# Optimization experiments

Measured on AMD Instinct MI355X. Metric: run time of the kernel, lower is better.

## Reference

```python
import jax, jax.numpy as jnp
import numpy as np

B, N, D, H, C = 16, 512, 256, 8, 16
DK = D // H  # per-head dim


def gelu(x):
    return jax.nn.gelu(x, approximate=False)  # torch F.gelu default (erf)


def mha(x, Wq, Wk, Wv, Wo):
    # x: [N, D] treated as a length-N token sequence; standard scaled-dot MHA
    n = x.shape[0]
    q = (x @ Wq).reshape(n, H, DK)
    k = (x @ Wk).reshape(n, H, DK)
    v = (x @ Wv).reshape(n, H, DK)
    scores = jnp.einsum('nhd,mhd->hnm', q, k) / jnp.sqrt(jnp.asarray(DK, x.dtype))
    attn = jax.nn.softmax(scores, axis=-1)
    out = jnp.einsum('hnm,mhd->nhd', attn, v).reshape(n, H * DK)
    return out @ Wo


def setup_inputs() -> dict:
    key = jax.random.key(0)
    ks = jax.random.split(key, 16)
    scale = 1.0 / np.sqrt(D)
    w = lambda i, shape: jax.random.normal(ks[i], shape, jnp.float32) * scale
    return {
        'embeddings': jax.random.normal(ks[0], (B, N, D), jnp.float32),
        'labels': jax.random.randint(ks[1], (B, N), 0, C),
        'Wq0': w(2, (D, D)), 'Wk0': w(3, (D, D)), 'Wv0': w(4, (D, D)), 'Wo0': w(5, (D, D)),
        'Wq1': w(6, (D, D)), 'Wk1': w(7, (D, D)), 'Wv1': w(8, (D, D)), 'Wo1': w(9, (D, D)),
        'res_W': w(10, (D, D)), 'res_b': jnp.zeros((D,), jnp.float32),
        'ff_W1': w(11, (2 * D, D)), 'ff_b1': jnp.zeros((D,), jnp.float32),
        'ff_W2': w(12, (D, D)), 'ff_b2': jnp.zeros((D,), jnp.float32),
    }


def reference(embeddings, labels, Wq0, Wk0, Wv0, Wo0, Wq1, Wk1, Wv1, Wo1,
              res_W, res_b, ff_W1, ff_b1, ff_W2, ff_b2):
    # one-hot class membership; torch.unique over randint labels == arange(C)
    onehot = (labels[..., None] == jnp.arange(C)).astype(jnp.float32)  # [B,N,C]

    def episode(e, m):
        # e: [N, D]  m: [N, C]
        x = mha(e, Wq0, Wk0, Wv0, Wo0)
        x = gelu(x)
        x = mha(x, Wq1, Wk1, Wv1, Wo1)
        aggr = gelu(jnp.mean(x, axis=0))          # [D]  set-level summary
        aggr = aggr @ res_W + res_b               # res_linear
        e2 = jnp.concatenate([jnp.broadcast_to(aggr, (N, D)), e], axis=1)  # [N,2D]
        e2 = gelu(e2)
        e2 = gelu(e2 @ ff_W1 + ff_b1) @ ff_W2 + ff_b2  # ff_linear -> [N,D]
        # pairwise sample similarities with self-exclusion
        S = e2 @ e2.T                              # [N,N]
        S = S * (1.0 - jnp.eye(N, dtype=S.dtype))
        counts = jnp.sum(m, axis=0)                # [C]
        norm = counts[None, :] - m                 # leave-one-out class size [N,C]
        return (S.T @ m) / norm                    # per-class masked mean -> [N,C]

    return jax.vmap(episode)(embeddings, onehot)
```

## Files before the change

### kernel.cpp

```cpp
#include <hip/hip_runtime.h>

#define BB 16
#define NN 512
#define DD 256
#define HH 8
#define CC 16

typedef unsigned short u16;
using short8 = __attribute__((ext_vector_type(8))) short;
using f32x4  = __attribute__((ext_vector_type(4))) float;

__device__ __forceinline__ float gelu_f(float x) {
    return 0.5f * x * (1.0f + erff(x * 0.70710678118654752f));
}
__device__ __forceinline__ u16 f2bf(float f) {
    unsigned int u = __float_as_uint(f);
    unsigned int r = u + 0x7FFFu + ((u >> 16) & 1u);
    return (u16)(r >> 16);
}
__device__ __forceinline__ void gld16(const u16* g, const u16* l) {
    __builtin_amdgcn_global_load_lds(
        (const __attribute__((address_space(1))) unsigned int*)g,
        (__attribute__((address_space(3))) unsigned int*)l, 16, 0, 0);
}

#define QSCALE 0.25505412f

template<int ACT, int HAS_B, int HAS_T, int OUT_F32>
__global__ __launch_bounds__(256) void gemm64(
    const u16* __restrict__ A, const u16* __restrict__ W,
    u16* __restrict__ O, float* __restrict__ OF,
    const float* __restrict__ bias, const float* __restrict__ tvec)
{
    __shared__ __align__(16) u16 As[64 * 32];
    __shared__ __align__(16) u16 Bs[64 * 32];
    const int tid = threadIdx.x, wave = tid >> 6, lane = tid & 63;
    const int col = lane & 15, quad = lane >> 4;
    const int mbase = blockIdx.x * 64;
    const int nbase = blockIdx.y * 64;
    const int srow = lane >> 2, skk = (lane & 3) * 8;
    const int mh = (wave & 1) * 32, nh = (wave >> 1) * 32;

    f32x4 acc[2][2];
#pragma unroll
    for (int i = 0; i < 2; ++i)
#pragma unroll
        for (int j = 0; j < 2; ++j) acc[i][j] = (f32x4){0.f, 0.f, 0.f, 0.f};

    for (int k0 = 0; k0 < DD; k0 += 32) {
        gld16(A + (size_t)(mbase + wave * 16 + srow) * DD + k0 + skk, &As[wave * 512]);
        gld16(W + (size_t)(nbase + wave * 16 + srow) * DD + k0 + skk, &Bs[wave * 512]);
        __syncthreads();
        short8 af[2], bfr[2];
#pragma unroll
        for (int i = 0; i < 2; ++i) af[i]  = *(const short8*)&As[(mh + i * 16 + col) * 32 + quad * 8];
#pragma unroll
        for (int j = 0; j < 2; ++j) bfr[j] = *(const short8*)&Bs[(nh + j * 16 + col) * 32 + quad * 8];
#pragma unroll
        for (int i = 0; i < 2; ++i)
#pragma unroll
            for (int j = 0; j < 2; ++j)
                acc[i][j] = __builtin_amdgcn_mfma_f32_16x16x32_bf16(af[i], bfr[j], acc[i][j], 0, 0, 0);
        __syncthreads();
    }

    const int b = mbase >> 9;
#pragma unroll
    for (int i = 0; i < 2; ++i) {
#pragma unroll
        for (int j = 0; j < 2; ++j) {
            const int ccol = nbase + nh + j * 16 + col;
#pragma unroll
            for (int r = 0; r < 4; ++r) {
                const int crow = mbase + mh + i * 16 + quad * 4 + r;
                float v = acc[i][j][r];
                if (HAS_B) v += bias[ccol];
                if (HAS_T) v += tvec[b * DD + ccol];
                if (ACT)   v = gelu_f(v);
                if (OUT_F32) OF[(size_t)crow * DD + ccol] = v;
                else         O[(size_t)crow * DD + ccol] = f2bf(v);
            }
        }
    }
}

__global__ __launch_bounds__(256) void gemm_qkv(
    const u16* __restrict__ A,
    const u16* __restrict__ W0, const u16* __restrict__ W1, const u16* __restrict__ W2,
    u16* __restrict__ O0, u16* __restrict__ O1, u16* __restrict__ O2)
{
    __shared__ __align__(16) u16 As[64 * 32];
    __shared__ __align__(16) u16 Bs[64 * 32];
    const int tid = threadIdx.x, wave = tid >> 6, lane = tid & 63;
    const int col = lane & 15, quad = lane >> 4;
    const int mbase = blockIdx.x * 64;
    const int sel = blockIdx.y >> 2;
    const int nbase = (blockIdx.y & 3) * 64;
    const u16* W = (sel == 0) ? W0 : ((sel == 1) ? W1 : W2);
    u16* O = (sel == 0) ? O0 : ((sel == 1) ? O1 : O2);
    const int srow = lane >> 2, skk = (lane & 3) * 8;
    const int mh = (wave & 1) * 32, nh = (wave >> 1) * 32;

    f32x4 acc[2][2];
#pragma unroll
    for (int i = 0; i < 2; ++i)
#pragma unroll
        for (int j = 0; j < 2; ++j) acc[i][j] = (f32x4){0.f, 0.f, 0.f, 0.f};

    for (int k0 = 0; k0 < DD; k0 += 32) {
        gld16(A + (size_t)(mbase + wave * 16 + srow) * DD + k0 + skk, &As[wave * 512]);
        gld16(W + (size_t)(nbase + wave * 16 + srow) * DD + k0 + skk, &Bs[wave * 512]);
        __syncthreads();
        short8 af[2], bfr[2];
#pragma unroll
        for (int i = 0; i < 2; ++i) af[i]  = *(const short8*)&As[(mh + i * 16 + col) * 32 + quad * 8];
#pragma unroll
        for (int j = 0; j < 2; ++j) bfr[j] = *(const short8*)&Bs[(nh + j * 16 + col) * 32 + quad * 8];
#pragma unroll
        for (int i = 0; i < 2; ++i)
#pragma unroll
            for (int j = 0; j < 2; ++j)
                acc[i][j] = __builtin_amdgcn_mfma_f32_16x16x32_bf16(af[i], bfr[j], acc[i][j], 0, 0, 0);
        __syncthreads();
    }

    const int b = mbase >> 9;
#pragma unroll
    for (int i = 0; i < 2; ++i) {
#pragma unroll
        for (int j = 0; j < 2; ++j) {
            const int ccol = nbase + nh + j * 16 + col;
            const int tok0 = (mbase & 511) + mh + i * 16 + quad * 4;
            const int head = ccol >> 5, dk = ccol & 31;
            if (sel == 2) {
                ushort4 pk;
                pk.x = f2bf(acc[i][j][0]); pk.y = f2bf(acc[i][j][1]);
                pk.z = f2bf(acc[i][j][2]); pk.w = f2bf(acc[i][j][3]);
                *(ushort4*)&O[(((size_t)b * HH + head) * 32 + dk) * NN + tok0] = pk;
            } else {
#pragma unroll
                for (int r = 0; r < 4; ++r) {
                    float v = acc[i][j][r];
                    if (sel == 0) v *= QSCALE;
                    O[(((size_t)b * HH + head) * NN + tok0 + r) * 32 + dk] = f2bf(v);
                }
            }
        }
    }
}

template<int COLSUM>
__global__ __launch_bounds__(256) void attn_mfma(
    const u16* __restrict__ Qh, const u16* __restrict__ Kh,
    const u16* __restrict__ VT, u16* __restrict__ O,
    float* __restrict__ partial)
{
    __shared__ __align__(16) u16 Vt[32 * 520];
    __shared__ __align__(16) u16 Pc[4][16 * 32];
    __shared__ float cs[4][32];
    const int tid = threadIdx.x, wave = tid >> 6, lane = tid & 63;
    const int col = lane & 15, quad = lane >> 4;
    const int gid = blockIdx.x;
    const int qb = gid >> 7, bh = gid & 127;
    const int q0 = qb * 64 + wave * 16;

    const u16* vsrc = VT + (size_t)bh * 32 * NN;
#pragma unroll
    for (int i = 0; i < 8; ++i) {
        const int row = wave + i * 4;
        gld16(vsrc + (size_t)row * NN + lane * 8, &Vt[row * 520]);
    }
    const short8 aq = *(const short8*)(Qh + ((size_t)bh * NN + q0 + col) * 32 + quad * 8);
    __syncthreads();

    const u16* ksrc = Kh + (size_t)bh * NN * 32;
    float l[4] = {0.f, 0.f, 0.f, 0.f};
    f32x4 oacc[2];
    oacc[0] = (f32x4){0.f, 0.f, 0.f, 0.f};
    oacc[1] = (f32x4){0.f, 0.f, 0.f, 0.f};

    for (int g = 0; g < 16; ++g) {
#pragma unroll
        for (int k2 = 0; k2 < 2; ++k2) {
            const int kt = g * 2 + k2;
            const short8 bk = *(const short8*)(ksrc + (size_t)(kt * 16 + col) * 32 + quad * 8);
            f32x4 z = {0.f, 0.f, 0.f, 0.f};
            const f32x4 s = __builtin_amdgcn_mfma_f32_16x16x32_bf16(aq, bk, z, 0, 0, 0);
#pragma unroll
            for (int r = 0; r < 4; ++r) {
                const float p = exp2f(s[r]);
                l[r] += p;
                Pc[wave][(quad * 4 + r) * 32 + k2 * 16 + col] = f2bf(p);
            }
        }
        const short8 ap = *(const short8*)&Pc[wave][col * 32 + quad * 8];
#pragma unroll
        for (int nt = 0; nt < 2; ++nt) {
            const short8 bv = *(const short8*)&Vt[(nt * 16 + col) * 520 + g * 32 + quad * 8];
            oacc[nt] = __builtin_amdgcn_mfma_f32_16x16x32_bf16(ap, bv, oacc[nt], 0, 0, 0);
        }
    }
#pragma unroll
    for (int r = 0; r < 4; ++r) {
        l[r] += __shfl_xor(l[r], 1, 64);
        l[r] += __shfl_xor(l[r], 2, 64);
        l[r] += __shfl_xor(l[r], 4, 64);
        l[r] += __shfl_xor(l[r], 8, 64);
    }
    if (COLSUM) {
        float sv[2] = {0.f, 0.f};
#pragma unroll
        for (int nt = 0; nt < 2; ++nt) {
#pragma unroll
            for (int r = 0; r < 4; ++r) sv[nt] += oacc[nt][r] / l[r];
            sv[nt] += __shfl_xor(sv[nt], 16, 64);
            sv[nt] += __shfl_xor(sv[nt], 32, 64);
        }
        if (lane < 16) { cs[wave][col] = sv[0]; cs[wave][16 + col] = sv[1]; }
        __syncthreads();
        if (tid < 32)
            partial[(size_t)(bh * 8 + qb) * 32 + tid] =
                cs[0][tid] + cs[1][tid] + cs[2][tid] + cs[3][tid];
    } else {
        const int b = bh >> 3, h = bh & 7;
        u16* obase = O + ((size_t)b * NN) * DD + h * 32;
#pragma unroll
        for (int nt = 0; nt < 2; ++nt)
#pragma unroll
            for (int r = 0; r < 4; ++r)
                obase[(size_t)(q0 + quad * 4 + r) * DD + nt * 16 + col] = f2bf(oacc[nt][r] / l[r]);
    }
}

__global__ __launch_bounds__(256) void convert_all(
    const float* __restrict__ e, u16* __restrict__ E, u16* __restrict__ G,
    const float* s0, const float* s1, const float* s2, const float* s3,
    const float* s4, const float* s5, const float* s6, const float* s7,
    const float* s8, u16* __restrict__ Wt)
{
    const int bx = blockIdx.x;
    if (bx < 2048) {
        const size_t i = ((size_t)bx * 256 + threadIdx.x) * 4;
        const float4 v = *(const float4*)(e + i);
        ushort4 ev, gv;
        ev.x = f2bf(v.x); ev.y = f2bf(v.y); ev.z = f2bf(v.z); ev.w = f2bf(v.w);
        gv.x = f2bf(gelu_f(v.x)); gv.y = f2bf(gelu_f(v.y));
        gv.z = f2bf(gelu_f(v.z)); gv.w = f2bf(gelu_f(v.w));
        *(ushort4*)(E + i) = ev;
        *(ushort4*)(G + i) = gv;
    } else {
        const int w = bx - 2048;
        const int my = w >> 4, kb = (w & 15) * 16;
        const int n = threadIdx.x;
        const float* S;
        switch (my) {
            case 0: S = s0; break; case 1: S = s1; break; case 2: S = s2; break;
            case 3: S = s3; break; case 4: S = s4; break; case 5: S = s5; break;
            case 6: S = s6; break; case 7: S = s7; break; default: S = s8; break;
        }
        u16* Dst = Wt + (size_t)my * 65536;
        for (int r = 0; r < 16; ++r) {
            const int k = kb + r;
            Dst[(size_t)n * 256 + k] = f2bf(S[(size_t)k * 256 + n]);
        }
    }
}

__device__ __forceinline__ float mv256(const float* __restrict__ a,
                                       const float* __restrict__ W, int d)
{
    float acc[8] = {0.f, 0.f, 0.f, 0.f, 0.f, 0.f, 0.f, 0.f};
    for (int k = 0; k < 256; k += 8) {
#pragma unroll
        for (int j = 0; j < 8; ++j)
            acc[j] += a[k + j] * W[(size_t)(k + j) * 256 + d];
    }
    return ((acc[0] + acc[1]) + (acc[2] + acc[3])) + ((acc[4] + acc[5]) + (acc[6] + acc[7]));
}

__global__ __launch_bounds__(256) void aggr_v2(
    const float* __restrict__ partial, const float* __restrict__ Wo1f,
    const float* __restrict__ resW, const float* __restrict__ resb,
    const float* __restrict__ W1, const int* __restrict__ labels,
    float* __restrict__ tvec, float* __restrict__ counts)
{
    const int b = blockIdx.x, d = threadIdx.x;
    __shared__ float a0[256], a1[256], a2[256];
    __shared__ int hist[CC];
    if (d < CC) hist[d] = 0;
    const int h = d >> 5, d32 = d & 31;
    float s = 0.f;
#pragma unroll
    for (int qb = 0; qb < 8; ++qb)
        s += partial[(size_t)(((b * 8 + h) * 8) + qb) * 32 + d32];
    a0[d] = s * (1.0f / NN);
    __syncthreads();
    atomicAdd(&hist[labels[b * NN + d]], 1);
    atomicAdd(&hist[labels[b * NN + 256 + d]], 1);
    a1[d] = gelu_f(mv256(a0, Wo1f, d));
    __syncthreads();
    a2[d] = gelu_f(mv256(a1, resW, d) + resb[d]);
    __syncthreads();
    tvec[b * 256 + d] = mv256(a2, W1, d);
    if (d < CC) counts[b * CC + d] = (float)hist[d];
}

__global__ __launch_bounds__(256) void classsum_v2(
    const float* __restrict__ F, const int* __restrict__ labels,
    float* __restrict__ g)
{
    const int b = blockIdx.x, dch = blockIdx.y;
    const int t = threadIdx.x, w = t >> 6, lane = t & 63;
    __shared__ int lab[NN];
    __shared__ float gs[4][CC][64];
    lab[t] = labels[b * NN + t];
    lab[t + 256] = labels[b * NN + t + 256];
    __syncthreads();
    float acc[CC];
#pragma unroll
    for (int c = 0; c < CC; ++c) acc[c] = 0.f;
    const float* Fb = F + (size_t)b * NN * DD + dch * 64 + lane;
#pragma unroll 4
    for (int n = w * 128; n < w * 128 + 128; ++n) {
        const float v = Fb[(size_t)n * DD];
        const int lb = lab[n];
#pragma unroll
        for (int c = 0; c < CC; ++c) acc[c] += (lb == c) ? v : 0.f;
    }
#pragma unroll
    for (int c = 0; c < CC; ++c) gs[w][c][lane] = acc[c];
    __syncthreads();
#pragma unroll
    for (int i = 0; i < 4; ++i) {
        const int c = w * 4 + i;
        g[((size_t)b * CC + c) * DD + dch * 64 + lane] =
            gs[0][c][lane] + gs[1][c][lane] + gs[2][c][lane] + gs[3][c][lane];
    }
}

__global__ __launch_bounds__(256) void out_kernel(
    const float* __restrict__ F, const int* __restrict__ labels,
    const float* __restrict__ g, const float* __restrict__ counts,
    float* __restrict__ out)
{
    const int b = blockIdx.y;
    const int wave = threadIdx.x >> 6, lane = threadIdx.x & 63;
    const int n = blockIdx.x * 4 + wave;
    const float* fn = F + ((size_t)b * NN + n) * DD;
    const float* gb = g + (size_t)b * CC * DD;
    float fv[4];
#pragma unroll
    for (int i = 0; i < 4; ++i) fv[i] = fn[lane * 4 + i];
    float selfdot = 0.f;
#pragma unroll
    for (int i = 0; i < 4; ++i) selfdot += fv[i] * fv[i];
    float accs[CC];
#pragma unroll
    for (int c = 0; c < CC; ++c) {
        float sacc = 0.f;
#pragma unroll
        for (int i = 0; i < 4; ++i) sacc += fv[i] * gb[c * DD + lane * 4 + i];
        accs[c] = sacc;
    }
    for (int off = 32; off; off >>= 1) {
        selfdot += __shfl_xor(selfdot, off, 64);
#pragma unroll
        for (int c = 0; c < CC; ++c) accs[c] += __shfl_xor(accs[c], off, 64);
    }
    if (lane < CC) {
        const int c = lane;
        const int same = (labels[b * NN + n] == c) ? 1 : 0;
        const float num = accs[c] - (same ? selfdot : 0.f);
        const float den = counts[b * CC + c] - (float)same;
        out[((size_t)b * NN + n) * CC + c] = num / den;
    }
}

extern "C" void kernel_launch(void* const* d_in, const int* in_sizes, int n_in,
                              void* d_out, int out_size, void* d_ws, size_t ws_size,
                              hipStream_t stream)
{
    const float* emb    = (const float*)d_in[0];
    const int*   labels = (const int*)  d_in[1];
    const float* Wo1f = (const float*)d_in[9];
    const float* resW = (const float*)d_in[10];
    const float* resb = (const float*)d_in[11];
    const float* ffW1 = (const float*)d_in[12];
    const float* ffb1 = (const float*)d_in[13];
    const float* ffb2 = (const float*)d_in[15];
    float* out = (float*)d_out;

    const size_t SBE = (size_t)BB * NN * DD;
    u16* BUF0 = (u16*)d_ws;
    u16* BUF1 = BUF0 + SBE;
    u16* BUF2 = BUF1 + SBE;
    u16* BUF3 = BUF2 + SBE;
    u16* BUF4 = BUF3 + SBE;
    u16* BUF5 = BUF4 + SBE;
    u16* Wt   = BUF5 + SBE;
    float* F      = (float*)(Wt + 9 * 65536);
    float* tvec   = F + SBE;
    float* partial= tvec + BB * 256;
    float* gsum   = partial + 128 * 8 * 32;
    float* counts = gsum + (size_t)BB * CC * DD;

    convert_all<<<2048 + 144, 256, 0, stream>>>(
        emb, BUF0, BUF1,
        (const float*)d_in[2], (const float*)d_in[3], (const float*)d_in[4],
        (const float*)d_in[5], (const float*)d_in[6], (const float*)d_in[7],
        (const float*)d_in[8], ffW1 + 256 * 256, (const float*)d_in[14], Wt);
    gemm_qkv<<<dim3(128, 12), 256, 0, stream>>>(
        BUF0, Wt, Wt + 65536, Wt + 2 * 65536, BUF2, BUF3, BUF4);
    attn_mfma<0><<<1024, 256, 0, stream>>>(BUF2, BUF3, BUF4, BUF5, nullptr);
    gemm64<1,0,0,0><<<dim3(128, 4), 256, 0, stream>>>(
        BUF5, Wt + 3 * 65536, BUF0, nullptr, nullptr, nullptr);
    gemm_qkv<<<dim3(128, 12), 256, 0, stream>>>(
        BUF0, Wt + 4 * 65536, Wt + 5 * 65536, Wt + 6 * 65536, BUF2, BUF3, BUF4);
    attn_mfma<1><<<1024, 256, 0, stream>>>(BUF2, BUF3, BUF4, nullptr, partial);
    aggr_v2<<<BB, 256, 0, stream>>>(partial, Wo1f, resW, resb, ffW1, labels, tvec, counts);
    gemm64<1,1,1,0><<<dim3(128, 4), 256, 0, stream>>>(
        BUF1, Wt + 7 * 65536, BUF3, nullptr, ffb1, tvec);
    gemm64<0,1,0,1><<<dim3(128, 4), 256, 0, stream>>>(
        BUF3, Wt + 8 * 65536, nullptr, F, ffb2, nullptr);
    classsum_v2<<<dim3(BB, 4), 256, 0, stream>>>(F, labels, gsum);
    out_kernel<<<dim3(128, BB), 256, 0, stream>>>(F, labels, gsum, counts, out);
}
```

Before: 211.2 us.

## Fuse embedding conversion into GEMM loaders, widen QKV tiles, drop V LDS staging

The standalone embedding fp32→bf16 and gelu conversion pass is removed. The first QKV GEMM now converts fp32 embeddings while loading them, and the FF1 GEMM applies gelu plus the bf16 conversion in its A-tile loader. The QKV GEMM tile grows to 128 rows to reuse each weight tile across more rows. Attention reads V straight from global memory instead of staging it in LDS, pads the P buffer and adds an occupancy bound, which trades LDS use for more global/L2 traffic.

```diff
diff --git a/kernel.cpp b/kernel.cpp
--- a/kernel.cpp
+++ b/kernel.cpp
@@ -26,98 +26,66 @@
 
 #define QSCALE 0.25505412f
 
-template<int ACT, int HAS_B, int HAS_T, int OUT_F32>
-__global__ __launch_bounds__(256) void gemm64(
-    const u16* __restrict__ A, const u16* __restrict__ W,
-    u16* __restrict__ O, float* __restrict__ OF,
-    const float* __restrict__ bias, const float* __restrict__ tvec)
-{
-    __shared__ __align__(16) u16 As[64 * 32];
+template<int AFP32>
+__global__ __launch_bounds__(256) void gemm_qkv128(
+    const void* __restrict__ Av,
+    const u16* __restrict__ W0, const u16* __restrict__ W1, const u16* __restrict__ W2,
+    u16* __restrict__ O0, u16* __restrict__ O1, u16* __restrict__ O2)
+{
+    __shared__ __align__(16) u16 As[128 * 32];
     __shared__ __align__(16) u16 Bs[64 * 32];
     const int tid = threadIdx.x, wave = tid >> 6, lane = tid & 63;
     const int col = lane & 15, quad = lane >> 4;
-    const int mbase = blockIdx.x * 64;
-    const int nbase = blockIdx.y * 64;
-    const int srow = lane >> 2, skk = (lane & 3) * 8;
-    const int mh = (wave & 1) * 32, nh = (wave >> 1) * 32;
-
-    f32x4 acc[2][2];
-#pragma unroll
-    for (int i = 0; i < 2; ++i)
-#pragma unroll
-        for (int j = 0; j < 2; ++j) acc[i][j] = (f32x4){0.f, 0.f, 0.f, 0.f};
-
-    for (int k0 = 0; k0 < DD; k0 += 32) {
-        gld16(A + (size_t)(mbase + wave * 16 + srow) * DD + k0 + skk, &As[wave * 512]);
-        gld16(W + (size_t)(nbase + wave * 16 + srow) * DD + k0 + skk, &Bs[wave * 512]);
-        __syncthreads();
-        short8 af[2], bfr[2];
-#pragma unroll
-        for (int i = 0; i < 2; ++i) af[i]  = *(const short8*)&As[(mh + i * 16 + col) * 32 + quad * 8];
-#pragma unroll
-        for (int j = 0; j < 2; ++j) bfr[j] = *(const short8*)&Bs[(nh + j * 16 + col) * 32 + quad * 8];
-#pragma unroll
-        for (int i = 0; i < 2; ++i)
-#pragma unroll
-            for (int j = 0; j < 2; ++j)
-                acc[i][j] = __builtin_amdgcn_mfma_f32_16x16x32_bf16(af[i], bfr[j], acc[i][j], 0, 0, 0);
-        __syncthreads();
-    }
-
-    const int b = mbase >> 9;
-#pragma unroll
-    for (int i = 0; i < 2; ++i) {
-#pragma unroll
-        for (int j = 0; j < 2; ++j) {
-            const int ccol = nbase + nh + j * 16 + col;
-#pragma unroll
-            for (int r = 0; r < 4; ++r) {
-                const int crow = mbase + mh + i * 16 + quad * 4 + r;
-                float v = acc[i][j][r];
-                if (HAS_B) v += bias[ccol];
-                if (HAS_T) v += tvec[b * DD + ccol];
-                if (ACT)   v = gelu_f(v);
-                if (OUT_F32) OF[(size_t)crow * DD + ccol] = v;
-                else         O[(size_t)crow * DD + ccol] = f2bf(v);
-            }
-        }
-    }
-}
-
-__global__ __launch_bounds__(256) void gemm_qkv(
-    const u16* __restrict__ A,
-    const u16* __restrict__ W0, const u16* __restrict__ W1, const u16* __restrict__ W2,
-    u16* __restrict__ O0, u16* __restrict__ O1, u16* __restrict__ O2)
-{
-    __shared__ __align__(16) u16 As[64 * 32];
-    __shared__ __align__(16) u16 Bs[64 * 32];
-    const int tid = threadIdx.x, wave = tid >> 6, lane = tid & 63;
-    const int col = lane & 15, quad = lane >> 4;
-    const int mbase = blockIdx.x * 64;
+    const int mbase = blockIdx.x * 128;
     const int sel = blockIdx.y >> 2;
     const int nbase = (blockIdx.y & 3) * 64;
     const u16* W = (sel == 0) ? W0 : ((sel == 1) ? W1 : W2);
     u16* O = (sel == 0) ? O0 : ((sel == 1) ? O1 : O2);
     const int srow = lane >> 2, skk = (lane & 3) * 8;
-    const int mh = (wave & 1) * 32, nh = (wave >> 1) * 32;
-
-    f32x4 acc[2][2];
-#pragma unroll
-    for (int i = 0; i < 2; ++i)
+    const int mh = (wave & 1) * 64, nh = (wave >> 1) * 32;
+
+    f32x4 acc[4][2];
+#pragma unroll
+    for (int i = 0; i < 4; ++i)
 #pragma unroll
         for (int j = 0; j < 2; ++j) acc[i][j] = (f32x4){0.f, 0.f, 0.f, 0.f};
 
     for (int k0 = 0; k0 < DD; k0 += 32) {
-        gld16(A + (size_t)(mbase + wave * 16 + srow) * DD + k0 + skk, &As[wave * 512]);
+        if (AFP32) {
+            const float* Af = (const float*)Av;
+            const int row = tid >> 1, half = tid & 1;
+            const float* src = Af + (size_t)(mbase + row) * DD + k0 + half * 16;
+            ushort4 w0, w1, w2, w3;
+            float4 v;
+            v = *(const float4*)(src + 0);
+            w0.x = f2bf(v.x); w0.y = f2bf(v.y); w0.z = f2bf(v.z); w0.w = f2bf(v.w);
+            v = *(const float4*)(src + 4);
+            w1.x = f2bf(v.x); w1.y = f2bf(v.y); w1.z = f2bf(v.z); w1.w = f2bf(v.w);
+            v = *(const float4*)(src + 8);
+            w2.x = f2bf(v.x); w2.y = f2bf(v.y); w2.z = f2bf(v.z); w2.w = f2bf(v.w);
+            v = *(const float4*)(src + 12);
+            w3.x = f2bf(v.x); w3.y = f2bf(v.y); w3.z = f2bf(v.z); w3.w = f2bf(v.w);
+            *(ushort4*)&As[row * 32 + half * 16 + 0]  = w0;
+            *(ushort4*)&As[row * 32 + half * 16 + 4]  = w1;
+            *(ushort4*)&As[row * 32 + half * 16 + 8]  = w2;
+            *(ushort4*)&As[row * 32 + half * 16 + 12] = w3;
+        } else {
+            const u16* Ab = (const u16*)Av;
+#pragma unroll
+            for (int c = 0; c < 2; ++c) {
+                const int ch = wave * 2 + c;
+                gld16(Ab + (size_t)(mbase + ch * 16 + srow) * DD + k0 + skk, &As[ch * 512]);
+            }
+        }
         gld16(W + (size_t)(nbase + wave * 16 + srow) * DD + k0 + skk, &Bs[wave * 512]);
         __syncthreads();
-        short8 af[2], bfr[2];
-#pragma unroll
-        for (int i = 0; i < 2; ++i) af[i]  = *(const short8*)&As[(mh + i * 16 + col) * 32 + quad * 8];
+        short8 af[4], bfr[2];
+#pragma unroll
+        for (int i = 0; i < 4; ++i) af[i]  = *(const short8*)&As[(mh + i * 16 + col) * 32 + quad * 8];
 #pragma unroll
         for (int j = 0; j < 2; ++j) bfr[j] = *(const short8*)&Bs[(nh + j * 16 + col) * 32 + quad * 8];
 #pragma unroll
-        for (int i = 0; i < 2; ++i)
+        for (int i = 0; i < 4; ++i)
 #pragma unroll
             for (int j = 0; j < 2; ++j)
                 acc[i][j] = __builtin_amdgcn_mfma_f32_16x16x32_bf16(af[i], bfr[j], acc[i][j], 0, 0, 0);
@@ -126,7 +94,7 @@
 
     const int b = mbase >> 9;
 #pragma unroll
-    for (int i = 0; i < 2; ++i) {
+    for (int i = 0; i < 4; ++i) {
 #pragma unroll
         for (int j = 0; j < 2; ++j) {
             const int ccol = nbase + nh + j * 16 + col;
@@ -149,14 +117,87 @@
     }
 }
 
+template<int ACT, int HAS_B, int HAS_T, int OUT_F32, int AG>
+__global__ __launch_bounds__(256) void gemm64(
+    const void* __restrict__ Av, const u16* __restrict__ W,
+    u16* __restrict__ O, float* __restrict__ OF,
+    const float* __restrict__ bias, const float* __restrict__ tvec)
+{
+    __shared__ __align__(16) u16 As[64 * 32];
+    __shared__ __align__(16) u16 Bs[64 * 32];
+    const int tid = threadIdx.x, wave = tid >> 6, lane = tid & 63;
+    const int col = lane & 15, quad = lane >> 4;
+    const int mbase = blockIdx.x * 64;
+    const int nbase = blockIdx.y * 64;
+    const int srow = lane >> 2, skk = (lane & 3) * 8;
+    const int mh = (wave & 1) * 32, nh = (wave >> 1) * 32;
+
+    f32x4 acc[2][2];
+#pragma unroll
+    for (int i = 0; i < 2; ++i)
+#pragma unroll
+        for (int j = 0; j < 2; ++j) acc[i][j] = (f32x4){0.f, 0.f, 0.f, 0.f};
+
+    for (int k0 = 0; k0 < DD; k0 += 32) {
+        if (AG) {
+            const float* Af = (const float*)Av;
+            const int row = tid >> 2, kq = tid & 3;
+            const float* src = Af + (size_t)(mbase + row) * DD + k0 + kq * 8;
+            float4 v0 = *(const float4*)(src + 0);
+            float4 v1 = *(const float4*)(src + 4);
+            ushort4 w0, w1;
+            w0.x = f2bf(gelu_f(v0.x)); w0.y = f2bf(gelu_f(v0.y));
+            w0.z = f2bf(gelu_f(v0.z)); w0.w = f2bf(gelu_f(v0.w));
+            w1.x = f2bf(gelu_f(v1.x)); w1.y = f2bf(gelu_f(v1.y));
+            w1.z = f2bf(gelu_f(v1.z)); w1.w = f2bf(gelu_f(v1.w));
+            *(ushort4*)&As[row * 32 + kq * 8 + 0] = w0;
+            *(ushort4*)&As[row * 32 + kq * 8 + 4] = w1;
+        } else {
+            const u16* Ab = (const u16*)Av;
+            gld16(Ab + (size_t)(mbase + wave * 16 + srow) * DD + k0 + skk, &As[wave * 512]);
+        }
+        gld16(W + (size_t)(nbase + wave * 16 + srow) * DD + k0 + skk, &Bs[wave * 512]);
+        __syncthreads();
+        short8 af[2], bfr[2];
+#pragma unroll
+        for (int i = 0; i < 2; ++i) af[i]  = *(const short8*)&As[(mh + i * 16 + col) * 32 + quad * 8];
+#pragma unroll
+        for (int j = 0; j < 2; ++j) bfr[j] = *(const short8*)&Bs[(nh + j * 16 + col) * 32 + quad * 8];
+#pragma unroll
+        for (int i = 0; i < 2; ++i)
+#pragma unroll
+            for (int j = 0; j < 2; ++j)
+                acc[i][j] = __builtin_amdgcn_mfma_f32_16x16x32_bf16(af[i], bfr[j], acc[i][j], 0, 0, 0);
+        __syncthreads();
+    }
+
+    const int b = mbase >> 9;
+#pragma unroll
+    for (int i = 0; i < 2; ++i) {
+#pragma unroll
+        for (int j = 0; j < 2; ++j) {
+            const int ccol = nbase + nh + j * 16 + col;
+#pragma unroll
+            for (int r = 0; r < 4; ++r) {
+                const int crow = mbase + mh + i * 16 + quad * 4 + r;
+                float v = acc[i][j][r];
+                if (HAS_B) v += bias[ccol];
+                if (HAS_T) v += tvec[b * DD + ccol];
+                if (ACT)   v = gelu_f(v);
+                if (OUT_F32) OF[(size_t)crow * DD + ccol] = v;
+                else         O[(size_t)crow * DD + ccol] = f2bf(v);
+            }
+        }
+    }
+}
+
 template<int COLSUM>
-__global__ __launch_bounds__(256) void attn_mfma(
+__global__ __launch_bounds__(256, 4) void attn_mfma(
     const u16* __restrict__ Qh, const u16* __restrict__ Kh,
     const u16* __restrict__ VT, u16* __restrict__ O,
     float* __restrict__ partial)
 {
-    __shared__ __align__(16) u16 Vt[32 * 520];
-    __shared__ __align__(16) u16 Pc[4][16 * 32];
+    __shared__ __align__(16) u16 Pc[4][16 * 40];
     __shared__ float cs[4][32];
     const int tid = threadIdx.x, wave = tid >> 6, lane = tid & 63;
     const int col = lane & 15, quad = lane >> 4;
@@ -164,21 +205,18 @@
     const int qb = gid >> 7, bh = gid & 127;
     const int q0 = qb * 64 + wave * 16;
 
+    const short8 aq = *(const short8*)(Qh + ((size_t)bh * NN + q0 + col) * 32 + quad * 8);
+    const u16* ksrc = Kh + (size_t)bh * NN * 32;
     const u16* vsrc = VT + (size_t)bh * 32 * NN;
-#pragma unroll
-    for (int i = 0; i < 8; ++i) {
-        const int row = wave + i * 4;
-        gld16(vsrc + (size_t)row * NN + lane * 8, &Vt[row * 520]);
-    }
-    const short8 aq = *(const short8*)(Qh + ((size_t)bh * NN + q0 + col) * 32 + quad * 8);
-    __syncthreads();
-
-    const u16* ksrc = Kh + (size_t)bh * NN * 32;
+
     float l[4] = {0.f, 0.f, 0.f, 0.f};
     f32x4 oacc[2];
     oacc[0] = (f32x4){0.f, 0.f, 0.f, 0.f};
     oacc[1] = (f32x4){0.f, 0.f, 0.f, 0.f};
 
+    u16* pw = &Pc[wave][0];
+
+#pragma unroll 4
     for (int g = 0; g < 16; ++g) {
 #pragma unroll
         for (int k2 = 0; k2 < 2; ++k2) {
@@ -190,13 +228,13 @@
             for (int r = 0; r < 4; ++r) {
                 const float p = exp2f(s[r]);
                 l[r] += p;
-                Pc[wave][(quad * 4 + r) * 32 + k2 * 16 + col] = f2bf(p);
+                pw[(quad * 4 + r) * 40 + k2 * 16 + col] = f2bf(p);
             }
         }
-        const short8 ap = *(const short8*)&Pc[wave][col * 32 + quad * 8];
+        const short8 ap = *(const short8*)&pw[col * 40 + quad * 8];
 #pragma unroll
         for (int nt = 0; nt < 2; ++nt) {
-            const short8 bv = *(const short8*)&Vt[(nt * 16 + col) * 520 + g * 32 + quad * 8];
+            const short8 bv = *(const short8*)(vsrc + (size_t)(nt * 16 + col) * NN + g * 32 + quad * 8);
             oacc[nt] = __builtin_amdgcn_mfma_f32_16x16x32_bf16(ap, bv, oacc[nt], 0, 0, 0);
         }
     }
@@ -232,37 +270,24 @@
     }
 }
 
-__global__ __launch_bounds__(256) void convert_all(
-    const float* __restrict__ e, u16* __restrict__ E, u16* __restrict__ G,
+__global__ __launch_bounds__(256) void convert_w(
     const float* s0, const float* s1, const float* s2, const float* s3,
     const float* s4, const float* s5, const float* s6, const float* s7,
     const float* s8, u16* __restrict__ Wt)
 {
-    const int bx = blockIdx.x;
-    if (bx < 2048) {
-        const size_t i = ((size_t)bx * 256 + threadIdx.x) * 4;
-        const float4 v = *(const float4*)(e + i);
-        ushort4 ev, gv;
-        ev.x = f2bf(v.x); ev.y = f2bf(v.y); ev.z = f2bf(v.z); ev.w = f2bf(v.w);
-        gv.x = f2bf(gelu_f(v.x)); gv.y = f2bf(gelu_f(v.y));
-        gv.z = f2bf(gelu_f(v.z)); gv.w = f2bf(gelu_f(v.w));
-        *(ushort4*)(E + i) = ev;
-        *(ushort4*)(G + i) = gv;
-    } else {
-        const int w = bx - 2048;
-        const int my = w >> 4, kb = (w & 15) * 16;
-        const int n = threadIdx.x;
-        const float* S;
-        switch (my) {
-            case 0: S = s0; break; case 1: S = s1; break; case 2: S = s2; break;
-            case 3: S = s3; break; case 4: S = s4; break; case 5: S = s5; break;
-            case 6: S = s6; break; case 7: S = s7; break; default: S = s8; break;
-        }
-        u16* Dst = Wt + (size_t)my * 65536;
-        for (int r = 0; r < 16; ++r) {
-            const int k = kb + r;
-            Dst[(size_t)n * 256 + k] = f2bf(S[(size_t)k * 256 + n]);
-        }
+    const int w = blockIdx.x;
+    const int my = w >> 4, kb = (w & 15) * 16;
+    const int n = threadIdx.x;
+    const float* S;
+    switch (my) {
+        case 0: S = s0; break; case 1: S = s1; break; case 2: S = s2; break;
+        case 3: S = s3; break; case 4: S = s4; break; case 5: S = s5; break;
+        case 6: S = s6; break; case 7: S = s7; break; default: S = s8; break;
+    }
+    u16* Dst = Wt + (size_t)my * 65536;
+    for (int r = 0; r < 16; ++r) {
+        const int k = kb + r;
+        Dst[(size_t)n * 256 + k] = f2bf(S[(size_t)k * 256 + n]);
     }
 }
 
@@ -392,8 +417,7 @@
 
     const size_t SBE = (size_t)BB * NN * DD;
     u16* BUF0 = (u16*)d_ws;
-    u16* BUF1 = BUF0 + SBE;
-    u16* BUF2 = BUF1 + SBE;
+    u16* BUF2 = BUF0 + SBE;
     u16* BUF3 = BUF2 + SBE;
     u16* BUF4 = BUF3 + SBE;
     u16* BUF5 = BUF4 + SBE;
@@ -404,23 +428,22 @@
     float* gsum   = partial + 128 * 8 * 32;
     float* counts = gsum + (size_t)BB * CC * DD;
 
-    convert_all<<<2048 + 144, 256, 0, stream>>>(
-        emb, BUF0, BUF1,
+    convert_w<<<144, 256, 0, stream>>>(
         (const float*)d_in[2], (const float*)d_in[3], (const float*)d_in[4],
         (const float*)d_in[5], (const float*)d_in[6], (const float*)d_in[7],
         (const float*)d_in[8], ffW1 + 256 * 256, (const float*)d_in[14], Wt);
-    gemm_qkv<<<dim3(128, 12), 256, 0, stream>>>(
-        BUF0, Wt, Wt + 65536, Wt + 2 * 65536, BUF2, BUF3, BUF4);
+    gemm_qkv128<1><<<dim3(64, 12), 256, 0, stream>>>(
+        emb, Wt, Wt + 65536, Wt + 2 * 65536, BUF2, BUF3, BUF4);
     attn_mfma<0><<<1024, 256, 0, stream>>>(BUF2, BUF3, BUF4, BUF5, nullptr);
-    gemm64<1,0,0,0><<<dim3(128, 4), 256, 0, stream>>>(
+    gemm64<1,0,0,0,0><<<dim3(128, 4), 256, 0, stream>>>(
         BUF5, Wt + 3 * 65536, BUF0, nullptr, nullptr, nullptr);
-    gemm_qkv<<<dim3(128, 12), 256, 0, stream>>>(
+    gemm_qkv128<0><<<dim3(64, 12), 256, 0, stream>>>(
         BUF0, Wt + 4 * 65536, Wt + 5 * 65536, Wt + 6 * 65536, BUF2, BUF3, BUF4);
     attn_mfma<1><<<1024, 256, 0, stream>>>(BUF2, BUF3, BUF4, nullptr, partial);
     aggr_v2<<<BB, 256, 0, stream>>>(partial, Wo1f, resW, resb, ffW1, labels, tvec, counts);
-    gemm64<1,1,1,0><<<dim3(128, 4), 256, 0, stream>>>(
-        BUF1, Wt + 7 * 65536, BUF3, nullptr, ffb1, tvec);
-    gemm64<0,1,0,1><<<dim3(128, 4), 256, 0, stream>>>(
+    gemm64<1,1,1,0,2><<<dim3(128, 4), 256, 0, stream>>>(
+        emb, Wt + 7 * 65536, BUF3, nullptr, ffb1, tvec);
+    gemm64<0,1,0,1,0><<<dim3(128, 4), 256, 0, stream>>>(
         BUF3, Wt + 8 * 65536, nullptr, F, ffb2, nullptr);
     classsum_v2<<<dim3(BB, 4), 256, 0, stream>>>(F, labels, gsum);
     out_kernel<<<dim3(128, BB), 256, 0, stream>>>(F, labels, gsum, counts, out);
```

Result: slower. 237.8 us (+12.6%).

## Fuse Q/K/V projections into one block sharing A tiles, deepen K step

Applied to the files above, without the earlier changes.

The QKV projection kernel now has each block compute all three outputs (Q, K, V) for its 64x64 tile. It loads the activation tile once and reuses it against three weight tiles, which cuts the grid from 1536 to 512 blocks and avoids re-reading A three times. Both GEMM kernels also stage two 32-wide K slices per barrier pair, halving the number of __syncthreads. The cost is more accumulator registers and LDS per block and fewer blocks in flight, which can lower occupancy.

```diff
diff --git a/kernel.cpp b/kernel.cpp
--- a/kernel.cpp
+++ b/kernel.cpp
@@ -26,20 +26,106 @@
 
 #define QSCALE 0.25505412f
 
-template<int ACT, int HAS_B, int HAS_T, int OUT_F32>
-__global__ __launch_bounds__(256) void gemm64(
-    const u16* __restrict__ A, const u16* __restrict__ W,
-    u16* __restrict__ O, float* __restrict__ OF,
-    const float* __restrict__ bias, const float* __restrict__ tvec)
-{
-    __shared__ __align__(16) u16 As[64 * 32];
-    __shared__ __align__(16) u16 Bs[64 * 32];
+__global__ __launch_bounds__(256) void gemm_qkv3(
+    const u16* __restrict__ A,
+    const u16* __restrict__ W0, const u16* __restrict__ W1, const u16* __restrict__ W2,
+    u16* __restrict__ O0, u16* __restrict__ O1, u16* __restrict__ O2)
+{
+    __shared__ __align__(16) u16 As[2][64 * 32];
+    __shared__ __align__(16) u16 Bs[3][2][64 * 32];
     const int tid = threadIdx.x, wave = tid >> 6, lane = tid & 63;
     const int col = lane & 15, quad = lane >> 4;
     const int mbase = blockIdx.x * 64;
     const int nbase = blockIdx.y * 64;
     const int srow = lane >> 2, skk = (lane & 3) * 8;
     const int mh = (wave & 1) * 32, nh = (wave >> 1) * 32;
+    const u16* Ws[3] = {W0, W1, W2};
+
+    f32x4 acc[3][2][2];
+#pragma unroll
+    for (int s = 0; s < 3; ++s)
+#pragma unroll
+        for (int i = 0; i < 2; ++i)
+#pragma unroll
+            for (int j = 0; j < 2; ++j) acc[s][i][j] = (f32x4){0.f, 0.f, 0.f, 0.f};
+
+    for (int k0 = 0; k0 < DD; k0 += 64) {
+#pragma unroll
+        for (int p = 0; p < 2; ++p) {
+            gld16(A + (size_t)(mbase + wave * 16 + srow) * DD + k0 + p * 32 + skk,
+                  &As[p][wave * 512]);
+#pragma unroll
+            for (int s = 0; s < 3; ++s)
+                gld16(Ws[s] + (size_t)(nbase + wave * 16 + srow) * DD + k0 + p * 32 + skk,
+                      &Bs[s][p][wave * 512]);
+        }
+        __syncthreads();
+#pragma unroll
+        for (int p = 0; p < 2; ++p) {
+            short8 af[2];
+#pragma unroll
+            for (int i = 0; i < 2; ++i)
+                af[i] = *(const short8*)&As[p][(mh + i * 16 + col) * 32 + quad * 8];
+#pragma unroll
+            for (int s = 0; s < 3; ++s) {
+                short8 bfr[2];
+#pragma unroll
+                for (int j = 0; j < 2; ++j)
+                    bfr[j] = *(const short8*)&Bs[s][p][(nh + j * 16 + col) * 32 + quad * 8];
+#pragma unroll
+                for (int i = 0; i < 2; ++i)
+#pragma unroll
+                    for (int j = 0; j < 2; ++j)
+                        acc[s][i][j] = __builtin_amdgcn_mfma_f32_16x16x32_bf16(
+                            af[i], bfr[j], acc[s][i][j], 0, 0, 0);
+            }
+        }
+        __syncthreads();
+    }
+
+    const int b = mbase >> 9;
+#pragma unroll
+    for (int s = 0; s < 3; ++s) {
+        u16* O = (s == 0) ? O0 : ((s == 1) ? O1 : O2);
+#pragma unroll
+        for (int i = 0; i < 2; ++i) {
+#pragma unroll
+            for (int j = 0; j < 2; ++j) {
+                const int ccol = nbase + nh + j * 16 + col;
+                const int tok0 = (mbase & 511) + mh + i * 16 + quad * 4;
+                const int head = ccol >> 5, dk = ccol & 31;
+                if (s == 2) {
+                    ushort4 pk;
+                    pk.x = f2bf(acc[s][i][j][0]); pk.y = f2bf(acc[s][i][j][1]);
+                    pk.z = f2bf(acc[s][i][j][2]); pk.w = f2bf(acc[s][i][j][3]);
+                    *(ushort4*)&O[(((size_t)b * HH + head) * 32 + dk) * NN + tok0] = pk;
+                } else {
+#pragma unroll
+                    for (int r = 0; r < 4; ++r) {
+                        float v = acc[s][i][j][r];
+                        if (s == 0) v *= QSCALE;
+                        O[(((size_t)b * HH + head) * NN + tok0 + r) * 32 + dk] = f2bf(v);
+                    }
+                }
+            }
+        }
+    }
+}
+
+template<int ACT, int HAS_B, int HAS_T, int OUT_F32>
+__global__ __launch_bounds__(256) void gemm64(
+    const u16* __restrict__ A, const u16* __restrict__ W,
+    u16* __restrict__ O, float* __restrict__ OF,
+    const float* __restrict__ bias, const float* __restrict__ tvec)
+{
+    __shared__ __align__(16) u16 As[2][64 * 32];
+    __shared__ __align__(16) u16 Bs[2][64 * 32];
+    const int tid = threadIdx.x, wave = tid >> 6, lane = tid & 63;
+    const int col = lane & 15, quad = lane >> 4;
+    const int mbase = blockIdx.x * 64;
+    const int nbase = blockIdx.y * 64;
+    const int srow = lane >> 2, skk = (lane & 3) * 8;
+    const int mh = (wave & 1) * 32, nh = (wave >> 1) * 32;
 
     f32x4 acc[2][2];
 #pragma unroll
@@ -47,20 +133,31 @@
 #pragma unroll
         for (int j = 0; j < 2; ++j) acc[i][j] = (f32x4){0.f, 0.f, 0.f, 0.f};
 
-    for (int k0 = 0; k0 < DD; k0 += 32) {
-        gld16(A + (size_t)(mbase + wave * 16 + srow) * DD + k0 + skk, &As[wave * 512]);
-        gld16(W + (size_t)(nbase + wave * 16 + srow) * DD + k0 + skk, &Bs[wave * 512]);
+    for (int k0 = 0; k0 < DD; k0 += 64) {
+#pragma unroll
+        for (int p = 0; p < 2; ++p) {
+            gld16(A + (size_t)(mbase + wave * 16 + srow) * DD + k0 + p * 32 + skk,
+                  &As[p][wave * 512]);
+            gld16(W + (size_t)(nbase + wave * 16 + srow) * DD + k0 + p * 32 + skk,
+                  &Bs[p][wave * 512]);
+        }
         __syncthreads();
-        short8 af[2], bfr[2];
-#pragma unroll
-        for (int i = 0; i < 2; ++i) af[i]  = *(const short8*)&As[(mh + i * 16 + col) * 32 + quad * 8];
-#pragma unroll
-        for (int j = 0; j < 2; ++j) bfr[j] = *(const short8*)&Bs[(nh + j * 16 + col) * 32 + quad * 8];
-#pragma unroll
-        for (int i = 0; i < 2; ++i)
+#pragma unroll
+        for (int p = 0; p < 2; ++p) {
+            short8 af[2], bfr[2];
+#pragma unroll
+            for (int i = 0; i < 2; ++i)
+                af[i] = *(const short8*)&As[p][(mh + i * 16 + col) * 32 + quad * 8];
 #pragma unroll
             for (int j = 0; j < 2; ++j)
-                acc[i][j] = __builtin_amdgcn_mfma_f32_16x16x32_bf16(af[i], bfr[j], acc[i][j], 0, 0, 0);
+                bfr[j] = *(const short8*)&Bs[p][(nh + j * 16 + col) * 32 + quad * 8];
+#pragma unroll
+            for (int i = 0; i < 2; ++i)
+#pragma unroll
+                for (int j = 0; j < 2; ++j)
+                    acc[i][j] = __builtin_amdgcn_mfma_f32_16x16x32_bf16(
+                        af[i], bfr[j], acc[i][j], 0, 0, 0);
+        }
         __syncthreads();
     }
 
@@ -79,71 +176,6 @@
                 if (ACT)   v = gelu_f(v);
                 if (OUT_F32) OF[(size_t)crow * DD + ccol] = v;
                 else         O[(size_t)crow * DD + ccol] = f2bf(v);
-            }
-        }
-    }
-}
-
-__global__ __launch_bounds__(256) void gemm_qkv(
-    const u16* __restrict__ A,
-    const u16* __restrict__ W0, const u16* __restrict__ W1, const u16* __restrict__ W2,
-    u16* __restrict__ O0, u16* __restrict__ O1, u16* __restrict__ O2)
-{
-    __shared__ __align__(16) u16 As[64 * 32];
-    __shared__ __align__(16) u16 Bs[64 * 32];
-    const int tid = threadIdx.x, wave = tid >> 6, lane = tid & 63;
-    const int col = lane & 15, quad = lane >> 4;
-    const int mbase = blockIdx.x * 64;
-    const int sel = blockIdx.y >> 2;
-    const int nbase = (blockIdx.y & 3) * 64;
-    const u16* W = (sel == 0) ? W0 : ((sel == 1) ? W1 : W2);
-    u16* O = (sel == 0) ? O0 : ((sel == 1) ? O1 : O2);
-    const int srow = lane >> 2, skk = (lane & 3) * 8;
-    const int mh = (wave & 1) * 32, nh = (wave >> 1) * 32;
-
-    f32x4 acc[2][2];
-#pragma unroll
-    for (int i = 0; i < 2; ++i)
-#pragma unroll
-        for (int j = 0; j < 2; ++j) acc[i][j] = (f32x4){0.f, 0.f, 0.f, 0.f};
-
-    for (int k0 = 0; k0 < DD; k0 += 32) {
-        gld16(A + (size_t)(mbase + wave * 16 + srow) * DD + k0 + skk, &As[wave * 512]);
-        gld16(W + (size_t)(nbase + wave * 16 + srow) * DD + k0 + skk, &Bs[wave * 512]);
-        __syncthreads();
-        short8 af[2], bfr[2];
-#pragma unroll
-        for (int i = 0; i < 2; ++i) af[i]  = *(const short8*)&As[(mh + i * 16 + col) * 32 + quad * 8];
-#pragma unroll
-        for (int j = 0; j < 2; ++j) bfr[j] = *(const short8*)&Bs[(nh + j * 16 + col) * 32 + quad * 8];
-#pragma unroll
-        for (int i = 0; i < 2; ++i)
-#pragma unroll
-            for (int j = 0; j < 2; ++j)
-                acc[i][j] = __builtin_amdgcn_mfma_f32_16x16x32_bf16(af[i], bfr[j], acc[i][j], 0, 0, 0);
-        __syncthreads();
-    }
-
-    const int b = mbase >> 9;
-#pragma unroll
-    for (int i = 0; i < 2; ++i) {
-#pragma unroll
-        for (int j = 0; j < 2; ++j) {
-            const int ccol = nbase + nh + j * 16 + col;
-            const int tok0 = (mbase & 511) + mh + i * 16 + quad * 4;
-            const int head = ccol >> 5, dk = ccol & 31;
-            if (sel == 2) {
-                ushort4 pk;
-                pk.x = f2bf(acc[i][j][0]); pk.y = f2bf(acc[i][j][1]);
-                pk.z = f2bf(acc[i][j][2]); pk.w = f2bf(acc[i][j][3]);
-                *(ushort4*)&O[(((size_t)b * HH + head) * 32 + dk) * NN + tok0] = pk;
-            } else {
-#pragma unroll
-                for (int r = 0; r < 4; ++r) {
-                    float v = acc[i][j][r];
-                    if (sel == 0) v *= QSCALE;
-                    O[(((size_t)b * HH + head) * NN + tok0 + r) * 32 + dk] = f2bf(v);
-                }
             }
         }
     }
@@ -409,12 +441,12 @@
         (const float*)d_in[2], (const float*)d_in[3], (const float*)d_in[4],
         (const float*)d_in[5], (const float*)d_in[6], (const float*)d_in[7],
         (const float*)d_in[8], ffW1 + 256 * 256, (const float*)d_in[14], Wt);
-    gemm_qkv<<<dim3(128, 12), 256, 0, stream>>>(
+    gemm_qkv3<<<dim3(128, 4), 256, 0, stream>>>(
         BUF0, Wt, Wt + 65536, Wt + 2 * 65536, BUF2, BUF3, BUF4);
     attn_mfma<0><<<1024, 256, 0, stream>>>(BUF2, BUF3, BUF4, BUF5, nullptr);
     gemm64<1,0,0,0><<<dim3(128, 4), 256, 0, stream>>>(
         BUF5, Wt + 3 * 65536, BUF0, nullptr, nullptr, nullptr);
-    gemm_qkv<<<dim3(128, 12), 256, 0, stream>>>(
+    gemm_qkv3<<<dim3(128, 4), 256, 0, stream>>>(
         BUF0, Wt + 4 * 65536, Wt + 5 * 65536, Wt + 6 * 65536, BUF2, BUF3, BUF4);
     attn_mfma<1><<<1024, 256, 0, stream>>>(BUF2, BUF3, BUF4, nullptr, partial);
     aggr_v2<<<BB, 256, 0, stream>>>(partial, Wo1f, resW, resb, ffW1, labels, tvec, counts);
```

Measured after the change: 214.2 us. No clear change (+1.4%).
